# Kernel tuning notes

Measured on AMD Instinct MI355X. Metric: run time of the kernel, lower is better.

The kernel has to match this reference:

```python
import jax, jax.numpy as jnp
import numpy as np

DIM = 1024
HEADS = 8


def setup_inputs() -> dict:
    key = jax.random.key(0)
    ks = jax.random.split(key, 8)
    b, n, m, nc, d = 2, 1024, 4, 1024, DIM
    x = jax.random.normal(ks[0], (b, n, d), dtype=jnp.float32)
    context = jax.random.normal(ks[1], (b, m, nc, d), dtype=jnp.float32)
    doc_similarities = jax.random.normal(ks[2], (b, m), dtype=jnp.float32)
    # learned params (Linear weights stored as [in, out] for x @ W)
    s = 1.0 / np.sqrt(d)
    Wq = jax.random.uniform(ks[3], (d, d), minval=-s, maxval=s, dtype=jnp.float32)
    Wkv = jax.random.uniform(ks[4], (d, 2 * d), minval=-s, maxval=s, dtype=jnp.float32)
    Wout = jax.random.uniform(ks[5], (d, d), minval=-s, maxval=s, dtype=jnp.float32)
    bout = jax.random.uniform(ks[6], (d,), minval=-s, maxval=s, dtype=jnp.float32)
    beta = jnp.array(1.0, dtype=jnp.float32)
    return {"x": x, "context": context, "doc_similarities": doc_similarities,
            "Wq": Wq, "Wkv": Wkv, "beta": beta, "Wout": Wout, "bout": bout}


def reference(x, context, doc_similarities, Wq, Wkv, beta, Wout, bout):
    b, n, dim = x.shape
    h = HEADS
    hd = dim // h
    scale = dim ** -0.5
    m, nc = context.shape[1], context.shape[2]

    # q: [b, h, n, hd]
    q = (x @ Wq).reshape(b, n, h, hd).transpose(0, 2, 1, 3)

    # flatten docs: [b, m*nc, dim]
    ctx = context.reshape(b, m * nc, dim)
    # doc similarity bias, repeated per token within each doc: [b, m*nc]
    sim = jnp.repeat(doc_similarities, nc, axis=1) * beta

    kv = ctx @ Wkv  # [b, L, 2*dim]
    k, v = jnp.split(kv, 2, axis=-1)
    k = k.reshape(b, m * nc, h, hd).transpose(0, 2, 1, 3)  # [b, h, L, hd]
    v = v.reshape(b, m * nc, h, hd).transpose(0, 2, 1, 3)

    dots = jnp.einsum('bhid,bhjd->bhij', q, k) * scale
    dots = dots + sim[:, None, None, :]
    attn = jax.nn.softmax(dots, axis=-1)
    out = jnp.einsum('bhij,bhjd->bhid', attn, v)
    out = out.transpose(0, 2, 1, 3).reshape(b, n, dim)
    return out @ Wout + bout
```

## Files before the change

### kernel.cpp

```cpp
#include <hip/hip_runtime.h>
#include <stdint.h>

typedef __attribute__((ext_vector_type(4))) float f32x4;
typedef __attribute__((ext_vector_type(8))) __bf16 bf16x8;

__device__ __forceinline__ uint16_t f2bf(float f) {
  uint32_t u = __builtin_bit_cast(uint32_t, f);
  u += 0x7FFFu + ((u >> 16) & 1u);
  return (uint16_t)(u >> 16);
}

__device__ __forceinline__ float bf2f(uint16_t u) {
  uint32_t v = ((uint32_t)u) << 16;
  return __builtin_bit_cast(float, v);
}

__device__ __forceinline__ void load_lds16(const uint16_t* g, uint16_t* l) {
  __builtin_amdgcn_global_load_lds((const __attribute__((address_space(1))) void*)g,
                                   (__attribute__((address_space(3))) void*)l, 16, 0, 0);
}

__global__ __launch_bounds__(256) void k_prep(const float* __restrict__ x,
                                              const float* __restrict__ ctx,
                                              const float* __restrict__ Wq,
                                              const float* __restrict__ Wkv,
                                              const float* __restrict__ Wout,
                                              uint16_t* __restrict__ xb,
                                              uint16_t* __restrict__ ctxb,
                                              uint16_t* __restrict__ wqt,
                                              uint16_t* __restrict__ wkvt,
                                              uint16_t* __restrict__ woutt,
                                              float qscale) {
  __shared__ float tile[32][33];
  int id = blockIdx.x;
  int tid = threadIdx.x;
  if (id < 10240) {
    const float* in;
    uint16_t* out;
    int j = id * 256 + tid;
    if (j < 524288) { in = x; out = xb; }
    else            { in = ctx; out = ctxb; j -= 524288; }
    float4 v = ((const float4*)in)[j];
    union { uint16_t u[4]; uint64_t q; } o;
    o.u[0] = f2bf(v.x); o.u[1] = f2bf(v.y); o.u[2] = f2bf(v.z); o.u[3] = f2bf(v.w);
    ((uint64_t*)out)[j] = o.q;
    return;
  }
  id -= 10240;
  const float* W;
  uint16_t* Wt;
  int N, n0, k0;
  float sc = 1.0f;
  if (id < 1024)      { W = Wq;   Wt = wqt;   N = 1024; sc = qscale;
                        n0 = (id & 31) * 32; k0 = (id >> 5) * 32; }
  else if (id < 2048) { W = Wout; Wt = woutt; N = 1024; id -= 1024;
                        n0 = (id & 31) * 32; k0 = (id >> 5) * 32; }
  else                { W = Wkv;  Wt = wkvt;  N = 2048; id -= 2048;
                        n0 = (id & 63) * 32; k0 = (id >> 6) * 32; }
  int c = tid & 31, r0 = tid >> 5;
#pragma unroll
  for (int i = 0; i < 4; i++) {
    int r = r0 + i * 8;
    tile[r][c] = W[(size_t)(k0 + r) * N + n0 + c];
  }
  __syncthreads();
#pragma unroll
  for (int i = 0; i < 4; i++) {
    int r = r0 + i * 8;
    Wt[(size_t)(n0 + r) * 1024 + k0 + c] = f2bf(tile[c][r] * sc);
  }
}

__global__ __launch_bounds__(256) void k_gemm_fused(const uint16_t* __restrict__ ctxb,
                                                    const uint16_t* __restrict__ wkvt,
                                                    const uint16_t* __restrict__ xb,
                                                    const uint16_t* __restrict__ wqt,
                                                    uint16_t* __restrict__ kb,
                                                    uint16_t* __restrict__ vtb,
                                                    uint16_t* __restrict__ qb) {
  __shared__ uint16_t smem[9216];
  uint16_t* la = smem;
  uint16_t* lb = smem + 4096;
  const int K = 1024;
  const int tid = threadIdx.x;
  const int lane = tid & 63, w = tid >> 6;
  const int quad = lane >> 4, l16 = lane & 15;
  const int wr = (w >> 1) * 64, wc = (w & 1) * 64;
  int id = blockIdx.x;
  int bx, by, isQ;
  const uint16_t *Ab, *Bb;
  if (id < 1024) {
    isQ = 0; bx = id & 15; by = id >> 4;
    Ab = ctxb + (size_t)by * 128 * K;
    Bb = wkvt + (size_t)bx * 128 * K;
  } else {
    isQ = 1; id -= 1024; bx = id & 7; by = id >> 3;
    Ab = xb + (size_t)by * 128 * K;
    Bb = wqt + (size_t)bx * 128 * K;
  }
  f32x4 acc[4][4] = {};
  const int rA = tid >> 2, slotA = tid & 3;
  const int rA1 = rA + 64;
  const int segA0 = (slotA ^ ((rA + (rA >> 2)) & 3)) * 8;
  const int segA1 = (slotA ^ ((rA1 + (rA1 >> 2)) & 3)) * 8;
  for (int k0 = 0; k0 < K; k0 += 32) {
    __syncthreads();
    load_lds16(Ab + (size_t)rA * K + k0 + segA0, la + tid * 8);
    load_lds16(Ab + (size_t)rA1 * K + k0 + segA1, la + (tid + 256) * 8);
    load_lds16(Bb + (size_t)rA * K + k0 + segA0, lb + tid * 8);
    load_lds16(Bb + (size_t)rA1 * K + k0 + segA1, lb + (tid + 256) * 8);
    __syncthreads();
    bf16x8 af[4], bfr[4];
#pragma unroll
    for (int i = 0; i < 4; i++) {
      int R = wr + i * 16 + l16;
      int s = quad ^ ((R + (R >> 2)) & 3);
      af[i] = *(const bf16x8*)&la[R * 32 + s * 8];
    }
#pragma unroll
    for (int j = 0; j < 4; j++) {
      int R = wc + j * 16 + l16;
      int s = quad ^ ((R + (R >> 2)) & 3);
      bfr[j] = *(const bf16x8*)&lb[R * 32 + s * 8];
    }
#pragma unroll
    for (int i = 0; i < 4; i++)
#pragma unroll
      for (int j = 0; j < 4; j++)
        acc[i][j] = __builtin_amdgcn_mfma_f32_16x16x32_bf16(af[i], bfr[j], acc[i][j], 0, 0, 0);
  }
  __syncthreads();
  if (isQ) {
#pragma unroll
    for (int i = 0; i < 4; i++)
#pragma unroll
      for (int j = 0; j < 4; j++) {
        size_t row = (size_t)by * 128 + wr + i * 16 + quad * 4;
        size_t col = (size_t)bx * 128 + wc + j * 16 + l16;
#pragma unroll
        for (int r = 0; r < 4; r++)
          qb[(row + r) * 1024 + col] = f2bf(acc[i][j][r]);
      }
  } else if (bx < 8) {
#pragma unroll
    for (int i = 0; i < 4; i++)
#pragma unroll
      for (int j = 0; j < 4; j++) {
        size_t row = (size_t)by * 128 + wr + i * 16 + quad * 4;
        size_t col = (size_t)bx * 128 + wc + j * 16 + l16;
#pragma unroll
        for (int r = 0; r < 4; r++)
          kb[(row + r) * 1024 + col] = f2bf(acc[i][j][r]);
      }
  } else {
    const int bh = (by >> 5) * 8 + (bx - 8);
    const int lbase = (by & 31) * 128;
    uint16_t* vdst = vtb + (size_t)bh * 524288;
#pragma unroll
    for (int half = 0; half < 2; half++) {
      if (wr == half * 64) {
#pragma unroll
        for (int i = 0; i < 4; i++)
#pragma unroll
          for (int j = 0; j < 4; j++) {
            int rowl = i * 16 + quad * 4;
            int col = wc + j * 16 + l16;
            union { uint64_t q; uint16_t u[4]; } pk;
#pragma unroll
            for (int r = 0; r < 4; r++) pk.u[r] = f2bf(acc[i][j][r]);
            *(uint64_t*)&smem[col * 72 + rowl] = pk.q;
          }
      }
      __syncthreads();
      {
        int col = tid >> 1, rseg = (tid & 1) * 32;
        const uint16_t* src = &smem[col * 72 + rseg];
        uint16_t* d = vdst + (size_t)col * 4096 + lbase + half * 64 + rseg;
#pragma unroll
        for (int k = 0; k < 4; k++)
          ((uint4*)d)[k] = *(const uint4*)&src[k * 8];
      }
      __syncthreads();
    }
  }
}

__global__ __launch_bounds__(256) void k_gemm64(const uint16_t* __restrict__ A,
                                                const uint16_t* __restrict__ Bt,
                                                float* __restrict__ Cf,
                                                const float* __restrict__ bias,
                                                int M, int N, int K) {
  __shared__ uint16_t la[64 * 64];
  __shared__ uint16_t lb[64 * 64];
  const int tid = threadIdx.x;
  const int lane = tid & 63, w = tid >> 6;
  const int quad = lane >> 4, l16 = lane & 15;
  const int wr = (w >> 1) * 32, wc = (w & 1) * 32;
  const size_t tr0 = (size_t)blockIdx.y * 64, tc0 = (size_t)blockIdx.x * 64;
  f32x4 acc[2][2] = {};
  const int rS = tid >> 3, sS = tid & 7;
  const int seg = (sS ^ (rS & 7)) * 8;
  const uint16_t* Ab = A + tr0 * K;
  const uint16_t* Bb = Bt + tc0 * K;
  for (int k0 = 0; k0 < K; k0 += 64) {
    __syncthreads();
    load_lds16(Ab + (size_t)rS * K + k0 + seg, la + tid * 8);
    load_lds16(Ab + (size_t)(rS + 32) * K + k0 + seg, la + (tid + 256) * 8);
    load_lds16(Bb + (size_t)rS * K + k0 + seg, lb + tid * 8);
    load_lds16(Bb + (size_t)(rS + 32) * K + k0 + seg, lb + (tid + 256) * 8);
    __syncthreads();
#pragma unroll
    for (int sub = 0; sub < 2; sub++) {
      const int kk = sub * 4 + quad;
      bf16x8 af[2], bfr[2];
#pragma unroll
      for (int i = 0; i < 2; i++) {
        int R = wr + i * 16 + l16;
        af[i] = *(const bf16x8*)&la[R * 64 + (kk ^ (R & 7)) * 8];
      }
#pragma unroll
      for (int j = 0; j < 2; j++) {
        int R = wc + j * 16 + l16;
        bfr[j] = *(const bf16x8*)&lb[R * 64 + (kk ^ (R & 7)) * 8];
      }
#pragma unroll
      for (int i = 0; i < 2; i++)
#pragma unroll
        for (int j = 0; j < 2; j++)
          acc[i][j] = __builtin_amdgcn_mfma_f32_16x16x32_bf16(af[i], bfr[j], acc[i][j], 0, 0, 0);
    }
  }
#pragma unroll
  for (int i = 0; i < 2; i++) {
#pragma unroll
    for (int j = 0; j < 2; j++) {
      size_t row = tr0 + wr + i * 16 + quad * 4;
      size_t col = tc0 + wc + j * 16 + l16;
#pragma unroll
      for (int r = 0; r < 4; r++)
        Cf[(row + r) * N + col] = acc[i][j][r] + bias[col];
    }
  }
}

__global__ __launch_bounds__(256) void k_attn(const uint16_t* __restrict__ q,
                                              const uint16_t* __restrict__ kb,
                                              const uint16_t* __restrict__ vt,
                                              const float* __restrict__ sims,
                                              const float* __restrict__ beta,
                                              uint16_t* __restrict__ po,
                                              float* __restrict__ pl) {
  __shared__ uint16_t Kl[8192];
  __shared__ uint16_t Vl[8192];
  __shared__ uint16_t Pl[4096];
  const int idx = blockIdx.x;
  const int qbx = idx >> 7, g = idx & 127;
  const int h = g >> 4, b = (g >> 3) & 1, sp = g & 7;
  const int q0 = qbx * 128;
  const int tid = threadIdx.x, lane = tid & 63, w = tid >> 6;
  const int quad = lane >> 4, l16 = lane & 15;
  const float wsplit =
      __builtin_amdgcn_exp2f(sims[b * 4 + (sp >> 1)] * beta[0] * 1.44269504f);
  uint16_t* Pw = Pl + w * 1024;

  union { uint32_t u[4]; bf16x8 v; } Oc;
#pragma unroll
  for (int j = 0; j < 4; j++) Oc.u[j] = 0x3F803F80u;
  const bf16x8 onesf = Oc.v;

  bf16x8 qf[2][4];
#pragma unroll
  for (int rb = 0; rb < 2; rb++) {
    const uint16_t* qrow =
        q + ((size_t)(b * 1024 + q0 + w * 32 + rb * 16 + l16)) * 1024 + h * 128 + quad * 8;
#pragma unroll
    for (int ks = 0; ks < 4; ks++) qf[rb][ks] = *(const bf16x8*)(qrow + ks * 32);
  }
  f32x4 o[2][8] = {};
  f32x4 o9[2] = {};

  const uint16_t* kptr = kb + ((size_t)(b * 4096 + sp * 512)) * 1024 + h * 128;
  const uint16_t* vptr = vt + ((size_t)(b * 8 + h) * 128) * 4096 + sp * 512;

  for (int c = 0; c < 8; c++) {
    __syncthreads();
#pragma unroll
    for (int ii = 0; ii < 4; ii++) {
      int g2 = tid + ii * 256;
      int row = g2 >> 4, seg = (g2 & 15) ^ (row & 15);
      load_lds16(kptr + (size_t)row * 1024 + seg * 8, Kl + g2 * 8);
    }
#pragma unroll
    for (int ii = 0; ii < 4; ii++) {
      int g2 = tid + ii * 256;
      int row = g2 >> 3, seg = (g2 & 7) ^ (row & 7);
      load_lds16(vptr + (size_t)row * 4096 + seg * 8, Vl + g2 * 8);
    }
    __syncthreads();
#pragma unroll
    for (int kh = 0; kh < 2; kh++) {
#pragma unroll
      for (int nb2 = 0; nb2 < 2; nb2++) {
        const int nb = kh * 2 + nb2;
        f32x4 s0 = {}, s1 = {};
#pragma unroll
        for (int ks = 0; ks < 4; ks++) {
          bf16x8 kf = *(const bf16x8*)&Kl[(nb * 16 + l16) * 128 + (((ks * 4 + quad) ^ l16) * 8)];
          s0 = __builtin_amdgcn_mfma_f32_16x16x32_bf16(qf[0][ks], kf, s0, 0, 0, 0);
          s1 = __builtin_amdgcn_mfma_f32_16x16x32_bf16(qf[1][ks], kf, s1, 0, 0, 0);
        }
        const int sl = nb2 * 2 + (l16 >> 3);
#pragma unroll
        for (int r = 0; r < 4; r++) {
          int rp0 = quad * 4 + r;
          Pw[rp0 * 32 + ((sl ^ ((rp0 >> 1) & 3)) * 8) + (l16 & 7)] =
              f2bf(__builtin_amdgcn_exp2f(s0[r]));
          int rp1 = 16 + rp0;
          Pw[rp1 * 32 + ((sl ^ ((rp1 >> 1) & 3)) * 8) + (l16 & 7)] =
              f2bf(__builtin_amdgcn_exp2f(s1[r]));
        }
      }
      __asm__ volatile("s_waitcnt lgkmcnt(0)" ::: "memory");
      const int segp = (quad ^ ((l16 >> 1) & 3)) * 8;
      bf16x8 pf0 = *(const bf16x8*)&Pw[l16 * 32 + segp];
      bf16x8 pf1 = *(const bf16x8*)&Pw[(16 + l16) * 32 + segp];
      const int sq = ((kh * 4 + quad) ^ (l16 & 7)) * 8;
#pragma unroll
      for (int nb = 0; nb < 8; nb++) {
        bf16x8 vf = *(const bf16x8*)&Vl[(nb * 16 + l16) * 64 + sq];
        o[0][nb] = __builtin_amdgcn_mfma_f32_16x16x32_bf16(pf0, vf, o[0][nb], 0, 0, 0);
        o[1][nb] = __builtin_amdgcn_mfma_f32_16x16x32_bf16(pf1, vf, o[1][nb], 0, 0, 0);
      }
      o9[0] = __builtin_amdgcn_mfma_f32_16x16x32_bf16(pf0, onesf, o9[0], 0, 0, 0);
      o9[1] = __builtin_amdgcn_mfma_f32_16x16x32_bf16(pf1, onesf, o9[1], 0, 0, 0);
    }
    kptr += (size_t)64 * 1024;
    vptr += 64;
  }
  const int rowbase = (sp * 16 + b * 8 + h) * 1024 + q0 + w * 32;
#pragma unroll
  for (int rb = 0; rb < 2; rb++)
#pragma unroll
    for (int r = 0; r < 4; r++) {
      int row = rowbase + rb * 16 + quad * 4 + r;
#pragma unroll
      for (int nb = 0; nb < 8; nb++)
        po[(size_t)row * 128 + nb * 16 + l16] = f2bf(o[rb][nb][r] * wsplit);
      if (l16 == 0)
        pl[row] = o9[rb][r] * wsplit;
    }
}

__global__ __launch_bounds__(256) void k_merge(const uint16_t* __restrict__ po,
                                               const float* __restrict__ pl,
                                               uint16_t* __restrict__ attb) {
  const int bq = blockIdx.x;
  const int b = bq >> 10, qi = bq & 1023;
  const int t = threadIdx.x;
  const int h = t >> 5, d0 = (t & 31) * 4;
  const int bh = b * 8 + h;
  float den = 0.f;
  float acc[4] = {0.f, 0.f, 0.f, 0.f};
#pragma unroll
  for (int s = 0; s < 8; s++) {
    den += pl[(s * 16 + bh) * 1024 + qi];
    union { uint64_t q; uint16_t u[4]; } v;
    v.q = *(const uint64_t*)&po[(((size_t)(s * 16 + bh)) * 1024 + qi) * 128 + d0];
#pragma unroll
    for (int j = 0; j < 4; j++) acc[j] += bf2f(v.u[j]);
  }
  const float inv = 1.0f / den;
  union { uint64_t q; uint16_t u[4]; } o;
#pragma unroll
  for (int j = 0; j < 4; j++) o.u[j] = f2bf(acc[j] * inv);
  *(uint64_t*)&attb[((size_t)(b * 1024 + qi)) * 1024 + h * 128 + d0] = o.q;
}

extern "C" void kernel_launch(void* const* d_in, const int* in_sizes, int n_in,
                              void* d_out, int out_size, void* d_ws, size_t ws_size,
                              hipStream_t stream) {
  (void)in_sizes; (void)n_in; (void)out_size; (void)ws_size;
  const float* x    = (const float*)d_in[0];
  const float* ctx  = (const float*)d_in[1];
  const float* sims = (const float*)d_in[2];
  const float* Wq   = (const float*)d_in[3];
  const float* Wkv  = (const float*)d_in[4];
  const float* beta = (const float*)d_in[5];
  const float* Wout = (const float*)d_in[6];
  const float* bout = (const float*)d_in[7];
  float* out = (float*)d_out;

  char* ws = (char*)d_ws;
  uint16_t* xb    = (uint16_t*)(ws + 0);
  uint16_t* ctxb  = (uint16_t*)(ws + (4u << 20));
  uint16_t* wqt   = (uint16_t*)(ws + (20u << 20));
  uint16_t* wkvt  = (uint16_t*)(ws + (22u << 20));
  uint16_t* kb    = (uint16_t*)(ws + (32u << 20));
  uint16_t* vtb   = (uint16_t*)(ws + (48u << 20));
  float*    pl    = (float*)   (ws + (64u << 20));
  uint16_t* woutt = (uint16_t*)(ws + (68u << 20));
  uint16_t* qb    = (uint16_t*)(ws + (70u << 20));
  uint16_t* attb  = (uint16_t*)(ws + (74u << 20));
  uint16_t* po = (uint16_t*)(ws + 0);

  const float LOG2E = 1.44269504f;
  const float qscale = 0.03125f * LOG2E;

  k_prep<<<14336, 256, 0, stream>>>(x, ctx, Wq, Wkv, Wout, xb, ctxb, wqt, wkvt, woutt, qscale);
  k_gemm_fused<<<1152, 256, 0, stream>>>(ctxb, wkvt, xb, wqt, kb, vtb, qb);
  k_attn<<<1024, 256, 0, stream>>>(qb, kb, vtb, sims, beta, po, pl);
  k_merge<<<2048, 256, 0, stream>>>(po, pl, attb);
  k_gemm64<<<dim3(16, 32), 256, 0, stream>>>(attb, woutt, out, bout, 2048, 1024, 1024);
}
```

Baseline: 231.9 us.

## Double GEMM K-tile to 64 with XOR swizzle and XCD-aware block remap

The fused QKV GEMM now stages 64-wide K slices in LDS instead of 32, which halves the number of barrier pairs per output tile and runs two MFMA sub-steps per stage. The LDS swizzle becomes a row-XOR over 8 slots to suit the wider rows. Block IDs are also remapped so consecutive blocks on the same XCD share A-row tiles, improving L2 reuse. LDS use grows to 32KB per block, which may lower occupancy.

```diff
diff --git a/kernel.cpp b/kernel.cpp
--- a/kernel.cpp
+++ b/kernel.cpp
@@ -78,9 +78,9 @@
                                                     uint16_t* __restrict__ kb,
                                                     uint16_t* __restrict__ vtb,
                                                     uint16_t* __restrict__ qb) {
-  __shared__ uint16_t smem[9216];
+  __shared__ uint16_t smem[16384];
   uint16_t* la = smem;
-  uint16_t* lb = smem + 4096;
+  uint16_t* lb = smem + 8192;
   const int K = 1024;
   const int tid = threadIdx.x;
   const int lane = tid & 63, w = tid >> 6;
@@ -90,44 +90,51 @@
   int bx, by, isQ;
   const uint16_t *Ab, *Bb;
   if (id < 1024) {
-    isQ = 0; bx = id & 15; by = id >> 4;
+    isQ = 0;
+    int xcd = id & 7, t = id >> 3;
+    by = (xcd << 3) + (t & 7);
+    bx = t >> 3;
     Ab = ctxb + (size_t)by * 128 * K;
     Bb = wkvt + (size_t)bx * 128 * K;
   } else {
-    isQ = 1; id -= 1024; bx = id & 7; by = id >> 3;
+    isQ = 1; id -= 1024;
+    int xcd = id & 7, t = id >> 3;
+    by = (xcd << 1) + (t & 1);
+    bx = t >> 1;
     Ab = xb + (size_t)by * 128 * K;
     Bb = wqt + (size_t)bx * 128 * K;
   }
   f32x4 acc[4][4] = {};
-  const int rA = tid >> 2, slotA = tid & 3;
-  const int rA1 = rA + 64;
-  const int segA0 = (slotA ^ ((rA + (rA >> 2)) & 3)) * 8;
-  const int segA1 = (slotA ^ ((rA1 + (rA1 >> 2)) & 3)) * 8;
-  for (int k0 = 0; k0 < K; k0 += 32) {
-    __syncthreads();
-    load_lds16(Ab + (size_t)rA * K + k0 + segA0, la + tid * 8);
-    load_lds16(Ab + (size_t)rA1 * K + k0 + segA1, la + (tid + 256) * 8);
-    load_lds16(Bb + (size_t)rA * K + k0 + segA0, lb + tid * 8);
-    load_lds16(Bb + (size_t)rA1 * K + k0 + segA1, lb + (tid + 256) * 8);
-    __syncthreads();
-    bf16x8 af[4], bfr[4];
-#pragma unroll
-    for (int i = 0; i < 4; i++) {
-      int R = wr + i * 16 + l16;
-      int s = quad ^ ((R + (R >> 2)) & 3);
-      af[i] = *(const bf16x8*)&la[R * 32 + s * 8];
-    }
-#pragma unroll
-    for (int j = 0; j < 4; j++) {
-      int R = wc + j * 16 + l16;
-      int s = quad ^ ((R + (R >> 2)) & 3);
-      bfr[j] = *(const bf16x8*)&lb[R * 32 + s * 8];
-    }
-#pragma unroll
-    for (int i = 0; i < 4; i++)
-#pragma unroll
-      for (int j = 0; j < 4; j++)
-        acc[i][j] = __builtin_amdgcn_mfma_f32_16x16x32_bf16(af[i], bfr[j], acc[i][j], 0, 0, 0);
+  for (int k0 = 0; k0 < K; k0 += 64) {
+    __syncthreads();
+#pragma unroll
+    for (int ii = 0; ii < 4; ii++) {
+      int g = tid + ii * 256;
+      int row = g >> 3, slot = g & 7, seg = (slot ^ (row & 7)) * 8;
+      load_lds16(Ab + (size_t)row * K + k0 + seg, la + g * 8);
+      load_lds16(Bb + (size_t)row * K + k0 + seg, lb + g * 8);
+    }
+    __syncthreads();
+#pragma unroll
+    for (int sub = 0; sub < 2; sub++) {
+      const int kk = sub * 4 + quad;
+      bf16x8 af[4], bfr[4];
+#pragma unroll
+      for (int i = 0; i < 4; i++) {
+        int R = wr + i * 16 + l16;
+        af[i] = *(const bf16x8*)&la[R * 64 + ((kk ^ (R & 7)) * 8)];
+      }
+#pragma unroll
+      for (int j = 0; j < 4; j++) {
+        int R = wc + j * 16 + l16;
+        bfr[j] = *(const bf16x8*)&lb[R * 64 + ((kk ^ (R & 7)) * 8)];
+      }
+#pragma unroll
+      for (int i = 0; i < 4; i++)
+#pragma unroll
+        for (int j = 0; j < 4; j++)
+          acc[i][j] = __builtin_amdgcn_mfma_f32_16x16x32_bf16(af[i], bfr[j], acc[i][j], 0, 0, 0);
+    }
   }
   __syncthreads();
   if (isQ) {
```

Measured after the change: 238.7 us. +2.9%, slower.
